# Optimization experiments

Measured on AMD Instinct MI355X. Metric: run time of the kernel, lower is better.

The kernel has to match this reference:

```python
import jax, jax.numpy as jnp
import numpy as np

TOPK = 10

def setup_inputs() -> dict:
    key = jax.random.key(0)
    k1, k2, k3, k4, k5 = jax.random.split(key, 5)
    B, N, M, d = 256, 64, 64, 32
    return {
        "featureVec": jax.random.normal(k1, (B, N, d), dtype=jnp.float32),
        "contextVec": jax.random.normal(k2, (B, M, d), dtype=jnp.float32),
        "Wq": jax.random.normal(k3, (d, d), dtype=jnp.float32) * 0.05,
        "Wk": jax.random.normal(k4, (d, d), dtype=jnp.float32) * 0.05,
        "Wv": jax.random.normal(k5, (d, M), dtype=jnp.float32) * 0.05,
    }


def _lambda_weight(featureVec, contextVec, Wq, Wk, Wv):
    # Lambda-attention producing weight [B, N, M] (M = contextFeatureNum).
    Q = jnp.einsum("bnd,dk->bnk", featureVec, Wq)                 # [B,N,k]
    K = jax.nn.softmax(jnp.einsum("bmd,dk->bmk", contextVec, Wk), axis=1)
    V = jnp.einsum("bmd,dv->bmv", contextVec, Wv)                 # [B,M,v=M]
    lam = jnp.einsum("bmk,bmv->bkv", K, V)                        # content lambda
    return jnp.einsum("bnk,bkv->bnv", Q, lam)                     # [B,N,M]


def reference(featureVec, contextVec, Wq, Wk, Wv):
    B, N, d = featureVec.shape
    # Outer-product value tensor [B, N, M, d]
    value = featureVec[:, :, None, :] * contextVec[:, None, :, :]
    weight = _lambda_weight(featureVec, contextVec, Wq, Wk, Wv)   # [B,N,M]
    topk_vals, idx = jax.lax.top_k(weight, TOPK)                  # [B,N,topk]
    topk_vals = jax.nn.softmax(topk_vals, axis=2)
    # Gather selected context slots along dim 2, then weighted combine.
    out = jnp.take_along_axis(value, idx[..., None], axis=2)      # [B,N,topk,d]
    out = topk_vals[..., None] * out
    return out.reshape(B, N * TOPK, d)
```

## Files before the change

### kernel.cpp

```cpp
#include <hip/hip_runtime.h>
#include <math.h>

constexpr int Bn = 256;
constexpr int Nn = 64;
constexpr int Mn = 64;
constexpr int Dn = 32;
constexpr int TK = 10;
constexpr int NT = 1024;

__device__ __forceinline__ float exp_np(float x) {
    return (float)exp((double)x);
}

__device__ __forceinline__ unsigned int f2u(float f) {
    unsigned int b = __float_as_uint(f);
    return (b & 0x80000000u) ? ~b : (b | 0x80000000u);
}
__device__ __forceinline__ float u2f(unsigned int u) {
    return __uint_as_float((u & 0x80000000u) ? (u ^ 0x80000000u) : ~u);
}

__global__ __launch_bounds__(NT) void sparse_lambda_attn_kernel(
    const float* __restrict__ fv,
    const float* __restrict__ cv,
    const float* __restrict__ Wq,
    const float* __restrict__ Wk,
    const float* __restrict__ Wv,
    float* __restrict__ out)
{
    #pragma clang fp contract(off)

    __shared__ float f_lds[Nn][Dn];
    __shared__ float c_lds[Mn][Dn];
    __shared__ float bufA[Mn][Dn];
    __shared__ float buf16[Mn][Mn + 1];
    __shared__ float lam[Dn][Mn];
    __shared__ float colmax[Dn];
    __shared__ float colsum[Dn];
    __shared__ float topw[Nn][TK];
    __shared__ int   topi[Nn][TK];

    const int b = blockIdx.x;
    const int tid = threadIdx.x;

    {
        const float4* f4 = reinterpret_cast<const float4*>(fv + (size_t)b * Nn * Dn);
        const float4* c4 = reinterpret_cast<const float4*>(cv + (size_t)b * Mn * Dn);
        float4* fl = reinterpret_cast<float4*>(&f_lds[0][0]);
        float4* cl = reinterpret_cast<float4*>(&c_lds[0][0]);
        if (tid < 512) fl[tid] = f4[tid];
        else           cl[tid - 512] = c4[tid - 512];
    }
    __syncthreads();

    for (int i = tid; i < Mn * Dn; i += NT) {
        const int m = i >> 5, k = i & 31;
        float acc = 0.f;
        for (int d = 0; d < Dn; ++d) {
            const float p = c_lds[m][d] * Wk[d * Dn + k];
            acc = acc + p;
        }
        bufA[m][k] = acc;
    }
    for (int i = tid; i < Mn * Mn; i += NT) {
        const int m = i >> 6, v = i & 63;
        float acc = 0.f;
        for (int d = 0; d < Dn; ++d) {
            const float p = c_lds[m][d] * Wv[d * Mn + v];
            acc = acc + p;
        }
        buf16[m][v] = acc;
    }
    __syncthreads();

    if (tid < Dn) {
        const int k = tid;
        float mx = bufA[0][k];
        for (int m = 1; m < Mn; ++m) mx = fmaxf(mx, bufA[m][k]);
        colmax[k] = mx;
    }
    __syncthreads();
    for (int i = tid; i < Mn * Dn; i += NT) {
        const int m = i >> 5, k = i & 31;
        bufA[m][k] = exp_np(bufA[m][k] - colmax[k]);
    }
    __syncthreads();
    if (tid < Dn) {
        const int k = tid;
        float s = 0.f;
        for (int m = 0; m < Mn; ++m) s = s + bufA[m][k];
        colsum[k] = s;
    }
    __syncthreads();
    for (int i = tid; i < Mn * Dn; i += NT) {
        const int m = i >> 5, k = i & 31;
        bufA[m][k] = bufA[m][k] / colsum[k];
    }
    __syncthreads();

    for (int i = tid; i < Dn * Mn; i += NT) {
        const int k = i >> 6, v = i & 63;
        float acc = 0.f;
        for (int m = 0; m < Mn; ++m) {
            const float p = bufA[m][k] * buf16[m][v];
            acc = acc + p;
        }
        lam[k][v] = acc;
    }
    __syncthreads();

    for (int i = tid; i < Nn * Dn; i += NT) {
        const int n = i >> 5, k = i & 31;
        float acc = 0.f;
        for (int d = 0; d < Dn; ++d) {
            const float p = f_lds[n][d] * Wq[d * Dn + k];
            acc = acc + p;
        }
        bufA[n][k] = acc;
    }
    __syncthreads();

    for (int i = tid; i < Nn * Mn; i += NT) {
        const int n = i >> 6, v = i & 63;
        float acc = 0.f;
        for (int k = 0; k < Dn; ++k) {
            const float p = bufA[n][k] * lam[k][v];
            acc = acc + p;
        }
        buf16[n][v] = acc;
    }
    __syncthreads();

    {
        const int lane = tid & 63;
        const int g    = tid & 15;
        const int n    = tid >> 4;

        float su0v; unsigned su0, su1, su2, su3;
        su0 = f2u(buf16[n][(g << 2) + 0]);
        su1 = f2u(buf16[n][(g << 2) + 1]);
        su2 = f2u(buf16[n][(g << 2) + 2]);
        su3 = f2u(buf16[n][(g << 2) + 3]);
        (void)su0v;
        unsigned avail = 0xFu;

        float val0 = 0.f, myval = 0.f;
        int   myidx = 0;

        #pragma unroll
        for (int t = 0; t < TK; ++t) {
            unsigned bu = 0u; int bm = 64;
            if ((avail & 1u) && su0 > bu) { bu = su0; bm = (g << 2) + 0; }
            if ((avail & 2u) && su1 > bu) { bu = su1; bm = (g << 2) + 1; }
            if ((avail & 4u) && su2 > bu) { bu = su2; bm = (g << 2) + 2; }
            if ((avail & 8u) && su3 > bu) { bu = su3; bm = (g << 2) + 3; }
            #pragma unroll
            for (int off = 1; off <= 8; off <<= 1) {
                const unsigned ou = __shfl_xor(bu, off);
                const int      om = __shfl_xor(bm, off);
                if (ou > bu || (ou == bu && om < bm)) { bu = ou; bm = om; }
            }
            const float bv = u2f(bu);
            if (t == 0) val0 = bv;
            if (g == t) { myval = bv; myidx = bm; }
            if ((bm >> 2) == g) avail &= ~(1u << (bm & 3));
        }

        const float ev_own = (g < TK) ? exp_np(myval - val0) : 0.f;
        float s = 0.f;
        #pragma unroll
        for (int t = 0; t < TK; ++t) {
            const float e = __shfl(ev_own, (lane & 48) + t);
            s = s + e;
        }
        if (g < TK) {
            topw[n][g] = ev_own / s;
            topi[n][g] = myidx;
        }
    }
    __syncthreads();

    float* ob = out + (size_t)b * (Nn * TK * Dn);
    constexpr int TOT4 = Nn * TK * Dn / 4;
    for (int i = tid; i < TOT4; i += NT) {
        const int n = i / (TK * Dn / 4);
        const int r = i - n * (TK * Dn / 4);
        const int t = r >> 3;
        const int d4 = r & 7;
        const float w = topw[n][t];
        const int m = topi[n][t];
        const float4 f4 = reinterpret_cast<const float4*>(&f_lds[n][0])[d4];
        const float4 c4 = reinterpret_cast<const float4*>(&c_lds[m][0])[d4];
        float4 o;
        { const float vx = f4.x * c4.x; o.x = w * vx; }
        { const float vy = f4.y * c4.y; o.y = w * vy; }
        { const float vz = f4.z * c4.z; o.z = w * vz; }
        { const float vw = f4.w * c4.w; o.w = w * vw; }
        reinterpret_cast<float4*>(ob)[i] = o;
    }
}

extern "C" void kernel_launch(void* const* d_in, const int* in_sizes, int n_in,
                              void* d_out, int out_size, void* d_ws, size_t ws_size,
                              hipStream_t stream) {
    const float* fv = (const float*)d_in[0];
    const float* cv = (const float*)d_in[1];
    const float* Wq = (const float*)d_in[2];
    const float* Wk = (const float*)d_in[3];
    const float* Wv = (const float*)d_in[4];
    float* out = (float*)d_out;

    sparse_lambda_attn_kernel<<<Bn, NT, 0, stream>>>(fv, cv, Wq, Wk, Wv, out);
}
```

Baseline: 28.13 us.

## Stage weights in LDS and register-block the small matmuls four outputs per thread

Wq, Wk and Wv are now copied into shared memory once per block instead of being read from global memory inside every inner loop. Each matmul stage has every thread compute four adjacent outputs using float4 LDS reads, and the Q projection now runs in the same phase as the K and V projections, which removes a barrier stage. The extra LDS arrays raise shared-memory use per block. The score buffer reuses Vw, with a barrier inside the final matmul so no thread overwrites Vw while others still read lam.

```diff
diff --git a/kernel.cpp b/kernel.cpp
--- a/kernel.cpp
+++ b/kernel.cpp
@@ -32,8 +32,12 @@
 
     __shared__ float f_lds[Nn][Dn];
     __shared__ float c_lds[Mn][Dn];
-    __shared__ float bufA[Mn][Dn];
-    __shared__ float buf16[Mn][Mn + 1];
+    __shared__ float wq[Dn][Dn];
+    __shared__ float wk[Dn][Dn];
+    __shared__ float wv[Dn][Mn];
+    __shared__ float Kp[Mn][Dn];
+    __shared__ float Qm[Nn][Dn];
+    __shared__ float Vw[Mn][Mn];
     __shared__ float lam[Dn][Mn];
     __shared__ float colmax[Dn];
     __shared__ float colsum[Dn];
@@ -44,90 +48,120 @@
     const int tid = threadIdx.x;
 
     {
-        const float4* f4 = reinterpret_cast<const float4*>(fv + (size_t)b * Nn * Dn);
-        const float4* c4 = reinterpret_cast<const float4*>(cv + (size_t)b * Mn * Dn);
-        float4* fl = reinterpret_cast<float4*>(&f_lds[0][0]);
-        float4* cl = reinterpret_cast<float4*>(&c_lds[0][0]);
-        if (tid < 512) fl[tid] = f4[tid];
-        else           cl[tid - 512] = c4[tid - 512];
-    }
-    __syncthreads();
-
+        const float4* F4 = reinterpret_cast<const float4*>(fv + (size_t)b * Nn * Dn);
+        const float4* C4 = reinterpret_cast<const float4*>(cv + (size_t)b * Mn * Dn);
+        const float4* Q4 = reinterpret_cast<const float4*>(Wq);
+        const float4* K4 = reinterpret_cast<const float4*>(Wk);
+        const float4* V4 = reinterpret_cast<const float4*>(Wv);
+        if (tid < 512) reinterpret_cast<float4*>(&f_lds[0][0])[tid] = F4[tid];
+        else           reinterpret_cast<float4*>(&c_lds[0][0])[tid - 512] = C4[tid - 512];
+        if (tid < 256)      reinterpret_cast<float4*>(&wq[0][0])[tid] = Q4[tid];
+        else if (tid < 512) reinterpret_cast<float4*>(&wk[0][0])[tid - 256] = K4[tid - 256];
+        else                reinterpret_cast<float4*>(&wv[0][0])[tid - 512] = V4[tid - 512];
+    }
+    __syncthreads();
+
+    {
+        if (tid < 512) {
+            const int m = tid >> 3, k4 = (tid & 7) << 2;
+            float a0 = 0.f, a1 = 0.f, a2 = 0.f, a3 = 0.f;
+            for (int d = 0; d < Dn; ++d) {
+                const float cc = c_lds[m][d];
+                const float4 w = *reinterpret_cast<const float4*>(&wk[d][k4]);
+                a0 = a0 + cc * w.x;
+                a1 = a1 + cc * w.y;
+                a2 = a2 + cc * w.z;
+                a3 = a3 + cc * w.w;
+            }
+            float4 r; r.x = a0; r.y = a1; r.z = a2; r.w = a3;
+            *reinterpret_cast<float4*>(&Kp[m][k4]) = r;
+        } else {
+            const int t = tid - 512;
+            const int n = t >> 3, k4 = (t & 7) << 2;
+            float a0 = 0.f, a1 = 0.f, a2 = 0.f, a3 = 0.f;
+            for (int d = 0; d < Dn; ++d) {
+                const float ff = f_lds[n][d];
+                const float4 w = *reinterpret_cast<const float4*>(&wq[d][k4]);
+                a0 = a0 + ff * w.x;
+                a1 = a1 + ff * w.y;
+                a2 = a2 + ff * w.z;
+                a3 = a3 + ff * w.w;
+            }
+            float4 r; r.x = a0; r.y = a1; r.z = a2; r.w = a3;
+            *reinterpret_cast<float4*>(&Qm[n][k4]) = r;
+        }
+        {
+            const int m = tid >> 4, v4 = (tid & 15) << 2;
+            float a0 = 0.f, a1 = 0.f, a2 = 0.f, a3 = 0.f;
+            for (int d = 0; d < Dn; ++d) {
+                const float cc = c_lds[m][d];
+                const float4 w = *reinterpret_cast<const float4*>(&wv[d][v4]);
+                a0 = a0 + cc * w.x;
+                a1 = a1 + cc * w.y;
+                a2 = a2 + cc * w.z;
+                a3 = a3 + cc * w.w;
+            }
+            float4 r; r.x = a0; r.y = a1; r.z = a2; r.w = a3;
+            *reinterpret_cast<float4*>(&Vw[m][v4]) = r;
+        }
+    }
+    __syncthreads();
+
+    if (tid < Dn) {
+        const int k = tid;
+        float mx = Kp[0][k];
+        for (int m = 1; m < Mn; ++m) mx = fmaxf(mx, Kp[m][k]);
+        colmax[k] = mx;
+    }
+    __syncthreads();
     for (int i = tid; i < Mn * Dn; i += NT) {
         const int m = i >> 5, k = i & 31;
-        float acc = 0.f;
-        for (int d = 0; d < Dn; ++d) {
-            const float p = c_lds[m][d] * Wk[d * Dn + k];
-            acc = acc + p;
-        }
-        bufA[m][k] = acc;
-    }
-    for (int i = tid; i < Mn * Mn; i += NT) {
-        const int m = i >> 6, v = i & 63;
-        float acc = 0.f;
-        for (int d = 0; d < Dn; ++d) {
-            const float p = c_lds[m][d] * Wv[d * Mn + v];
-            acc = acc + p;
-        }
-        buf16[m][v] = acc;
-    }
-    __syncthreads();
-
-    if (tid < Dn) {
-        const int k = tid;
-        float mx = bufA[0][k];
-        for (int m = 1; m < Mn; ++m) mx = fmaxf(mx, bufA[m][k]);
-        colmax[k] = mx;
-    }
-    __syncthreads();
-    for (int i = tid; i < Mn * Dn; i += NT) {
-        const int m = i >> 5, k = i & 31;
-        bufA[m][k] = exp_np(bufA[m][k] - colmax[k]);
+        Kp[m][k] = exp_np(Kp[m][k] - colmax[k]);
     }
     __syncthreads();
     if (tid < Dn) {
         const int k = tid;
         float s = 0.f;
-        for (int m = 0; m < Mn; ++m) s = s + bufA[m][k];
+        for (int m = 0; m < Mn; ++m) s = s + Kp[m][k];
         colsum[k] = s;
     }
     __syncthreads();
     for (int i = tid; i < Mn * Dn; i += NT) {
         const int m = i >> 5, k = i & 31;
-        bufA[m][k] = bufA[m][k] / colsum[k];
-    }
-    __syncthreads();
-
-    for (int i = tid; i < Dn * Mn; i += NT) {
-        const int k = i >> 6, v = i & 63;
-        float acc = 0.f;
+        Kp[m][k] = Kp[m][k] / colsum[k];
+    }
+    __syncthreads();
+
+    if (tid < 512) {
+        const int k = tid >> 4, v4 = (tid & 15) << 2;
+        float a0 = 0.f, a1 = 0.f, a2 = 0.f, a3 = 0.f;
         for (int m = 0; m < Mn; ++m) {
-            const float p = bufA[m][k] * buf16[m][v];
-            acc = acc + p;
-        }
-        lam[k][v] = acc;
-    }
-    __syncthreads();
-
-    for (int i = tid; i < Nn * Dn; i += NT) {
-        const int n = i >> 5, k = i & 31;
-        float acc = 0.f;
-        for (int d = 0; d < Dn; ++d) {
-            const float p = f_lds[n][d] * Wq[d * Dn + k];
-            acc = acc + p;
-        }
-        bufA[n][k] = acc;
-    }
-    __syncthreads();
-
-    for (int i = tid; i < Nn * Mn; i += NT) {
-        const int n = i >> 6, v = i & 63;
-        float acc = 0.f;
+            const float kk = Kp[m][k];
+            const float4 vv = *reinterpret_cast<const float4*>(&Vw[m][v4]);
+            a0 = a0 + kk * vv.x;
+            a1 = a1 + kk * vv.y;
+            a2 = a2 + kk * vv.z;
+            a3 = a3 + kk * vv.w;
+        }
+        float4 r; r.x = a0; r.y = a1; r.z = a2; r.w = a3;
+        *reinterpret_cast<float4*>(&lam[k][v4]) = r;
+    }
+    __syncthreads();
+
+    {
+        const int n = tid >> 4, v4 = (tid & 15) << 2;
+        float a0 = 0.f, a1 = 0.f, a2 = 0.f, a3 = 0.f;
         for (int k = 0; k < Dn; ++k) {
-            const float p = bufA[n][k] * lam[k][v];
-            acc = acc + p;
-        }
-        buf16[n][v] = acc;
+            const float qq = Qm[n][k];
+            const float4 ll = *reinterpret_cast<const float4*>(&lam[k][v4]);
+            a0 = a0 + qq * ll.x;
+            a1 = a1 + qq * ll.y;
+            a2 = a2 + qq * ll.z;
+            a3 = a3 + qq * ll.w;
+        }
+        __syncthreads();
+        float4 r; r.x = a0; r.y = a1; r.z = a2; r.w = a3;
+        *reinterpret_cast<float4*>(&Vw[n][v4]) = r;
     }
     __syncthreads();
 
@@ -136,12 +170,8 @@
         const int g    = tid & 15;
         const int n    = tid >> 4;
 
-        float su0v; unsigned su0, su1, su2, su3;
-        su0 = f2u(buf16[n][(g << 2) + 0]);
-        su1 = f2u(buf16[n][(g << 2) + 1]);
-        su2 = f2u(buf16[n][(g << 2) + 2]);
-        su3 = f2u(buf16[n][(g << 2) + 3]);
-        (void)su0v;
+        const float4 s4 = *reinterpret_cast<const float4*>(&Vw[n][g << 2]);
+        unsigned su0 = f2u(s4.x), su1 = f2u(s4.y), su2 = f2u(s4.z), su3 = f2u(s4.w);
         unsigned avail = 0xFu;
 
         float val0 = 0.f, myval = 0.f;
```

Result: faster. 24.70 us (-12.2%).

## Register-tile the small GEMMs with transposed LDS operands and merged projections

Applied to the files above, without the earlier changes.

Stores transposed copies of the feature and context tiles in shared memory and computes the K, V and Q projections in one combined phase. Wave-uniform weight reads are hoisted, and the column max comes from a wavefront shuffle reduction instead of a serial loop. The lambda and weight GEMMs now use 4x4 register tiles with float4 LDS reads over padded arrays. This cuts shared-memory traffic, bank conflicts and barriers, but leaves only 128 and 256 threads active in those two GEMM phases and raises LDS use.

```diff
diff --git a/kernel.cpp b/kernel.cpp
--- a/kernel.cpp
+++ b/kernel.cpp
@@ -7,11 +7,11 @@
 constexpr int Dn = 32;
 constexpr int TK = 10;
 constexpr int NT = 1024;
+constexpr int PAD = 68;
 
 __device__ __forceinline__ float exp_np(float x) {
     return (float)exp((double)x);
 }
-
 __device__ __forceinline__ unsigned int f2u(float f) {
     unsigned int b = __float_as_uint(f);
     return (b & 0x80000000u) ? ~b : (b | 0x80000000u);
@@ -32,116 +32,172 @@
 
     __shared__ float f_lds[Nn][Dn];
     __shared__ float c_lds[Mn][Dn];
-    __shared__ float bufA[Mn][Dn];
-    __shared__ float buf16[Mn][Mn + 1];
-    __shared__ float lam[Dn][Mn];
-    __shared__ float colmax[Dn];
-    __shared__ float colsum[Dn];
+    __shared__ float fT[Dn][Nn];
+    __shared__ float cT[Dn][Mn];
+    __shared__ float KpT[Dn][PAD];
+    __shared__ float QmT[Dn][PAD];
+    __shared__ float Vw[Mn][PAD];
+    __shared__ float lamS[Dn][PAD];
+    __shared__ float Wt[Nn][PAD];
+    __shared__ float colmax[Dn], colsum[Dn];
     __shared__ float topw[Nn][TK];
     __shared__ int   topi[Nn][TK];
 
-    const int b = blockIdx.x;
-    const int tid = threadIdx.x;
-
-    {
-        const float4* f4 = reinterpret_cast<const float4*>(fv + (size_t)b * Nn * Dn);
-        const float4* c4 = reinterpret_cast<const float4*>(cv + (size_t)b * Mn * Dn);
-        float4* fl = reinterpret_cast<float4*>(&f_lds[0][0]);
-        float4* cl = reinterpret_cast<float4*>(&c_lds[0][0]);
-        if (tid < 512) fl[tid] = f4[tid];
-        else           cl[tid - 512] = c4[tid - 512];
-    }
-    __syncthreads();
-
-    for (int i = tid; i < Mn * Dn; i += NT) {
-        const int m = i >> 5, k = i & 31;
-        float acc = 0.f;
+    const int b    = blockIdx.x;
+    const int tid  = threadIdx.x;
+    const int lane = tid & 63;
+    const int wid  = tid >> 6;
+
+    if (tid < 512) {
+        const float4 v = reinterpret_cast<const float4*>(fv + (size_t)b * Nn * Dn)[tid];
+        const int n = tid >> 3, d4 = (tid & 7) << 2;
+        *reinterpret_cast<float4*>(&f_lds[n][d4]) = v;
+        fT[d4 + 0][n] = v.x; fT[d4 + 1][n] = v.y; fT[d4 + 2][n] = v.z; fT[d4 + 3][n] = v.w;
+    } else {
+        const int t = tid - 512;
+        const float4 v = reinterpret_cast<const float4*>(cv + (size_t)b * Mn * Dn)[t];
+        const int m = t >> 3, d4 = (t & 7) << 2;
+        *reinterpret_cast<float4*>(&c_lds[m][d4]) = v;
+        cT[d4 + 0][m] = v.x; cT[d4 + 1][m] = v.y; cT[d4 + 2][m] = v.z; cT[d4 + 3][m] = v.w;
+    }
+    __syncthreads();
+
+    if (wid < 8) {
+        const int kq = __builtin_amdgcn_readfirstlane(wid);
+        const int m = lane;
+        const float* wkq = Wk + (kq << 2);
+        const float* wvq = Wv + (kq << 3);
+        float a0=0.f,a1=0.f,a2=0.f,a3=0.f;
+        float b0=0.f,b1=0.f,b2=0.f,b3=0.f,b4=0.f,b5=0.f,b6=0.f,b7=0.f;
+        #pragma unroll 4
         for (int d = 0; d < Dn; ++d) {
-            const float p = c_lds[m][d] * Wk[d * Dn + k];
-            acc = acc + p;
-        }
-        bufA[m][k] = acc;
-    }
-    for (int i = tid; i < Mn * Mn; i += NT) {
-        const int m = i >> 6, v = i & 63;
-        float acc = 0.f;
+            const float cc = cT[d][m];
+            const float* wr = wkq + d * Dn;
+            const float* ur = wvq + d * Mn;
+            const float w0 = wr[0], w1 = wr[1], w2 = wr[2], w3 = wr[3];
+            const float u0 = ur[0], u1 = ur[1], u2 = ur[2], u3 = ur[3];
+            const float u4 = ur[4], u5 = ur[5], u6 = ur[6], u7 = ur[7];
+            a0 = a0 + cc * w0;  a1 = a1 + cc * w1;  a2 = a2 + cc * w2;  a3 = a3 + cc * w3;
+            b0 = b0 + cc * u0;  b1 = b1 + cc * u1;  b2 = b2 + cc * u2;  b3 = b3 + cc * u3;
+            b4 = b4 + cc * u4;  b5 = b5 + cc * u5;  b6 = b6 + cc * u6;  b7 = b7 + cc * u7;
+        }
+        KpT[(kq << 2) + 0][m] = a0;
+        KpT[(kq << 2) + 1][m] = a1;
+        KpT[(kq << 2) + 2][m] = a2;
+        KpT[(kq << 2) + 3][m] = a3;
+        float m0=a0, m1=a1, m2=a2, m3=a3;
+        #pragma unroll
+        for (int off = 1; off < 64; off <<= 1) {
+            m0 = fmaxf(m0, __shfl_xor(m0, off));
+            m1 = fmaxf(m1, __shfl_xor(m1, off));
+            m2 = fmaxf(m2, __shfl_xor(m2, off));
+            m3 = fmaxf(m3, __shfl_xor(m3, off));
+        }
+        if (lane == 0) {
+            colmax[(kq << 2) + 0] = m0;
+            colmax[(kq << 2) + 1] = m1;
+            colmax[(kq << 2) + 2] = m2;
+            colmax[(kq << 2) + 3] = m3;
+        }
+        float4 r0; r0.x = b0; r0.y = b1; r0.z = b2; r0.w = b3;
+        float4 r1; r1.x = b4; r1.y = b5; r1.z = b6; r1.w = b7;
+        *reinterpret_cast<float4*>(&Vw[m][(kq << 3) + 0]) = r0;
+        *reinterpret_cast<float4*>(&Vw[m][(kq << 3) + 4]) = r1;
+    } else {
+        const int qq = __builtin_amdgcn_readfirstlane(wid - 8);
+        const int n = lane;
+        const float* wqq = Wq + (qq << 2);
+        float a0=0.f,a1=0.f,a2=0.f,a3=0.f;
+        #pragma unroll 4
         for (int d = 0; d < Dn; ++d) {
-            const float p = c_lds[m][d] * Wv[d * Mn + v];
-            acc = acc + p;
-        }
-        buf16[m][v] = acc;
-    }
-    __syncthreads();
-
-    if (tid < Dn) {
-        const int k = tid;
-        float mx = bufA[0][k];
-        for (int m = 1; m < Mn; ++m) mx = fmaxf(mx, bufA[m][k]);
-        colmax[k] = mx;
-    }
-    __syncthreads();
-    for (int i = tid; i < Mn * Dn; i += NT) {
-        const int m = i >> 5, k = i & 31;
-        bufA[m][k] = exp_np(bufA[m][k] - colmax[k]);
+            const float ff = fT[d][n];
+            const float* wr = wqq + d * Dn;
+            const float w0 = wr[0], w1 = wr[1], w2 = wr[2], w3 = wr[3];
+            a0 = a0 + ff * w0;  a1 = a1 + ff * w1;  a2 = a2 + ff * w2;  a3 = a3 + ff * w3;
+        }
+        QmT[(qq << 2) + 0][n] = a0;
+        QmT[(qq << 2) + 1][n] = a1;
+        QmT[(qq << 2) + 2][n] = a2;
+        QmT[(qq << 2) + 3][n] = a3;
+    }
+    __syncthreads();
+
+    for (int i = tid; i < Dn * Mn; i += NT) {
+        const int k = i >> 6, m = i & 63;
+        KpT[k][m] = exp_np(KpT[k][m] - colmax[k]);
     }
     __syncthreads();
     if (tid < Dn) {
         const int k = tid;
         float s = 0.f;
-        for (int m = 0; m < Mn; ++m) s = s + bufA[m][k];
+        for (int m = 0; m < Mn; ++m) s = s + KpT[k][m];
         colsum[k] = s;
     }
     __syncthreads();
-    for (int i = tid; i < Mn * Dn; i += NT) {
-        const int m = i >> 5, k = i & 31;
-        bufA[m][k] = bufA[m][k] / colsum[k];
-    }
-    __syncthreads();
-
     for (int i = tid; i < Dn * Mn; i += NT) {
-        const int k = i >> 6, v = i & 63;
-        float acc = 0.f;
+        const int k = i >> 6, m = i & 63;
+        KpT[k][m] = KpT[k][m] / colsum[k];
+    }
+    __syncthreads();
+
+    if (tid < 128) {
+        const int kb = (tid >> 4) << 2;
+        const int v4 = (tid & 15) << 2;
+        float a00=0.f,a01=0.f,a02=0.f,a03=0.f;
+        float a10=0.f,a11=0.f,a12=0.f,a13=0.f;
+        float a20=0.f,a21=0.f,a22=0.f,a23=0.f;
+        float a30=0.f,a31=0.f,a32=0.f,a33=0.f;
         for (int m = 0; m < Mn; ++m) {
-            const float p = bufA[m][k] * buf16[m][v];
-            acc = acc + p;
-        }
-        lam[k][v] = acc;
-    }
-    __syncthreads();
-
-    for (int i = tid; i < Nn * Dn; i += NT) {
-        const int n = i >> 5, k = i & 31;
-        float acc = 0.f;
-        for (int d = 0; d < Dn; ++d) {
-            const float p = f_lds[n][d] * Wq[d * Dn + k];
-            acc = acc + p;
-        }
-        bufA[n][k] = acc;
-    }
-    __syncthreads();
-
-    for (int i = tid; i < Nn * Mn; i += NT) {
-        const int n = i >> 6, v = i & 63;
-        float acc = 0.f;
+            const float k0 = KpT[kb + 0][m];
+            const float k1 = KpT[kb + 1][m];
+            const float k2 = KpT[kb + 2][m];
+            const float k3 = KpT[kb + 3][m];
+            const float4 vv = *reinterpret_cast<const float4*>(&Vw[m][v4]);
+            a00 = a00 + k0 * vv.x;  a01 = a01 + k0 * vv.y;  a02 = a02 + k0 * vv.z;  a03 = a03 + k0 * vv.w;
+            a10 = a10 + k1 * vv.x;  a11 = a11 + k1 * vv.y;  a12 = a12 + k1 * vv.z;  a13 = a13 + k1 * vv.w;
+            a20 = a20 + k2 * vv.x;  a21 = a21 + k2 * vv.y;  a22 = a22 + k2 * vv.z;  a23 = a23 + k2 * vv.w;
+            a30 = a30 + k3 * vv.x;  a31 = a31 + k3 * vv.y;  a32 = a32 + k3 * vv.z;  a33 = a33 + k3 * vv.w;
+        }
+        float4 r;
+        r.x=a00; r.y=a01; r.z=a02; r.w=a03; *reinterpret_cast<float4*>(&lamS[kb+0][v4]) = r;
+        r.x=a10; r.y=a11; r.z=a12; r.w=a13; *reinterpret_cast<float4*>(&lamS[kb+1][v4]) = r;
+        r.x=a20; r.y=a21; r.z=a22; r.w=a23; *reinterpret_cast<float4*>(&lamS[kb+2][v4]) = r;
+        r.x=a30; r.y=a31; r.z=a32; r.w=a33; *reinterpret_cast<float4*>(&lamS[kb+3][v4]) = r;
+    }
+    __syncthreads();
+
+    if (tid < 256) {
+        const int nb = (tid >> 4) << 2;
+        const int v4 = (tid & 15) << 2;
+        float a00=0.f,a01=0.f,a02=0.f,a03=0.f;
+        float a10=0.f,a11=0.f,a12=0.f,a13=0.f;
+        float a20=0.f,a21=0.f,a22=0.f,a23=0.f;
+        float a30=0.f,a31=0.f,a32=0.f,a33=0.f;
         for (int k = 0; k < Dn; ++k) {
-            const float p = bufA[n][k] * lam[k][v];
-            acc = acc + p;
-        }
-        buf16[n][v] = acc;
+            const float q0 = QmT[k][nb + 0];
+            const float q1 = QmT[k][nb + 1];
+            const float q2 = QmT[k][nb + 2];
+            const float q3 = QmT[k][nb + 3];
+            const float4 lv = *reinterpret_cast<const float4*>(&lamS[k][v4]);
+            a00 = a00 + q0 * lv.x;  a01 = a01 + q0 * lv.y;  a02 = a02 + q0 * lv.z;  a03 = a03 + q0 * lv.w;
+            a10 = a10 + q1 * lv.x;  a11 = a11 + q1 * lv.y;  a12 = a12 + q1 * lv.z;  a13 = a13 + q1 * lv.w;
+            a20 = a20 + q2 * lv.x;  a21 = a21 + q2 * lv.y;  a22 = a22 + q2 * lv.z;  a23 = a23 + q2 * lv.w;
+            a30 = a30 + q3 * lv.x;  a31 = a31 + q3 * lv.y;  a32 = a32 + q3 * lv.z;  a33 = a33 + q3 * lv.w;
+        }
+        float4 r;
+        r.x=a00; r.y=a01; r.z=a02; r.w=a03; *reinterpret_cast<float4*>(&Wt[nb+0][v4]) = r;
+        r.x=a10; r.y=a11; r.z=a12; r.w=a13; *reinterpret_cast<float4*>(&Wt[nb+1][v4]) = r;
+        r.x=a20; r.y=a21; r.z=a22; r.w=a23; *reinterpret_cast<float4*>(&Wt[nb+2][v4]) = r;
+        r.x=a30; r.y=a31; r.z=a32; r.w=a33; *reinterpret_cast<float4*>(&Wt[nb+3][v4]) = r;
     }
     __syncthreads();
 
     {
-        const int lane = tid & 63;
-        const int g    = tid & 15;
-        const int n    = tid >> 4;
-
-        float su0v; unsigned su0, su1, su2, su3;
-        su0 = f2u(buf16[n][(g << 2) + 0]);
-        su1 = f2u(buf16[n][(g << 2) + 1]);
-        su2 = f2u(buf16[n][(g << 2) + 2]);
-        su3 = f2u(buf16[n][(g << 2) + 3]);
-        (void)su0v;
+        const int g = tid & 15;
+        const int n = tid >> 4;
+
+        const float4 s4 = *reinterpret_cast<const float4*>(&Wt[n][g << 2]);
+        unsigned su0 = f2u(s4.x), su1 = f2u(s4.y), su2 = f2u(s4.z), su3 = f2u(s4.w);
         unsigned avail = 0xFu;
 
         float val0 = 0.f, myval = 0.f;
```

New measurement: 26.22 us. -6.8%, faster.
